# Kernel tuning notes

Measured on AMD Instinct MI355X. Metric: run time of the kernel, lower is better.

## Reference

```python
import jax, jax.numpy as jnp
import numpy as np

EMBED_DIM = 1024
CONTEXT_LEN = 2048
NUM_HEADS = 16
HEAD_DIM = EMBED_DIM // NUM_HEADS
BATCH = 2
SEQ = 2048


def setup_inputs() -> dict:
    key = jax.random.key(0)
    ks = jax.random.split(key, 6)
    s = 1.0 / np.sqrt(EMBED_DIM)
    x = jax.random.normal(ks[0], (BATCH, SEQ, EMBED_DIM), dtype=jnp.float32)
    # nn.Linear weights stored as [out, in]; we keep [in, out] for x @ W
    W_q = jax.random.uniform(ks[1], (EMBED_DIM, EMBED_DIM), jnp.float32, -s, s)
    W_k = jax.random.uniform(ks[2], (EMBED_DIM, EMBED_DIM), jnp.float32, -s, s)
    W_v = jax.random.uniform(ks[3], (EMBED_DIM, EMBED_DIM), jnp.float32, -s, s)
    W_o = jax.random.uniform(ks[4], (EMBED_DIM, EMBED_DIM), jnp.float32, -s, s)
    b_o = jax.random.uniform(ks[5], (EMBED_DIM,), jnp.float32, -s, s)
    return {"x": x, "W_q": W_q, "W_k": W_k, "W_v": W_v, "W_o": W_o, "b_o": b_o}


def reference(x, W_q, W_k, W_v, W_o, b_o):
    b, s, _ = x.shape
    # project and split heads: [b, s, e] -> [b, h, s, d]
    def heads(t):
        return t.reshape(b, s, NUM_HEADS, HEAD_DIM).transpose(0, 2, 1, 3)
    q = heads(x @ W_q)
    k = heads(x @ W_k)
    v = heads(x @ W_v)
    scores = jnp.einsum("bhqd,bhkd->bhqk", q, k)  # full seq x seq scores
    causal = jnp.triu(jnp.ones((s, s), dtype=bool), k=1)
    scores = jnp.where(causal, -jnp.inf, scores)
    attn = jax.nn.softmax(scores / np.sqrt(HEAD_DIM).astype(np.float32), axis=-1)
    ctx = jnp.einsum("bhqk,bhkd->bhqd", attn, v)
    ctx = ctx.transpose(0, 2, 1, 3).reshape(b, s, EMBED_DIM)
    return ctx @ W_o + b_o
```

## Files before the change

### kernel.cpp

```cpp
#include <hip/hip_runtime.h>

#define EMBED 1024
#define SEQL  2048
#define NHEAD 16
#define HDIM  64
#define NBATCH 2
#define MROWS 4096

typedef __attribute__((ext_vector_type(4))) float  f32x4;
typedef __attribute__((ext_vector_type(8))) __bf16 bf16x8;

__device__ __forceinline__ short f2bf(float f){
  union { float f; unsigned u; } x; x.f = f;
  unsigned r = x.u + 0x7fffu + ((x.u >> 16) & 1u);
  return (short)(r >> 16);
}

#define GLDS(gp, lp) __builtin_amdgcn_global_load_lds( \
    (const __attribute__((address_space(1))) void*)(gp), \
    (__attribute__((address_space(3))) void*)(lp), 16, 0, 0)

__global__ __launch_bounds__(256) void cvt_kernel(const float* __restrict__ in,
                                                  short* __restrict__ out, int n){
  int i = (blockIdx.x * 256 + threadIdx.x) * 4;
  if (i >= n) return;
  float4 v = *(const float4*)(in + i);
  short4 o; o.x = f2bf(v.x); o.y = f2bf(v.y); o.z = f2bf(v.z); o.w = f2bf(v.w);
  *(short4*)(out + i) = o;
}

__global__ __launch_bounds__(256) void transpose_kernel(const float* __restrict__ W0,
    const float* __restrict__ W1, const float* __restrict__ W2, const float* __restrict__ W3,
    short* __restrict__ WtAll){
  __shared__ float tile[32][33];
  const int z = blockIdx.z;
  const float* W = (z==0)?W0:(z==1)?W1:(z==2)?W2:W3;
  short* Wt = WtAll + z*(EMBED*EMBED);
  const int bx = blockIdx.x*32, by = blockIdx.y*32;
  const int tx = threadIdx.x & 31, ty = threadIdx.x >> 5;
  #pragma unroll
  for (int i=0;i<32;i+=8) tile[ty+i][tx] = W[(by+ty+i)*EMBED + bx+tx];
  __syncthreads();
  #pragma unroll
  for (int i=0;i<32;i+=8) Wt[(bx+ty+i)*EMBED + by+tx] = f2bf(tile[tx][ty+i]);
}

__device__ __forceinline__ void gemm_tile_128(const short* __restrict__ A,
    const short* __restrict__ Bt, short* As, short* Bs, int m0, int n0, f32x4 acc[4][4]){
  const int tid  = threadIdx.x;
  const int lane = tid & 63;
  const int wid  = tid >> 6;
  const int wrow = (wid >> 1) * 64, wcol = (wid & 1) * 64;
  const int arow = tid >> 2, acol8 = (tid & 3) * 8;
  const int l15 = lane & 15, lg = lane >> 4;

  auto STAGE = [&](int b, int k0){
    short* as = As + b*4096;
    short* bs = Bs + b*4096;
    GLDS(A  + (m0      + arow) * 1024 + k0 + acol8, as + tid*8);
    GLDS(A  + (m0 + 64 + arow) * 1024 + k0 + acol8, as + 2048 + tid*8);
    GLDS(Bt + (n0      + arow) * 1024 + k0 + acol8, bs + tid*8);
    GLDS(Bt + (n0 + 64 + arow) * 1024 + k0 + acol8, bs + 2048 + tid*8);
  };

  STAGE(0, 0);
  __syncthreads();
  int cur = 0;
  for (int k0 = 0; k0 < 1024; k0 += 32){
    if (k0 + 32 < 1024) STAGE(cur ^ 1, k0 + 32);
    const short* as = As + cur*4096;
    const short* bs = Bs + cur*4096;
    bf16x8 a[4], b[4];
    #pragma unroll
    for (int i=0;i<4;++i) a[i] = *(const bf16x8*)(as + (wrow+16*i+l15)*32 + 8*lg);
    #pragma unroll
    for (int j=0;j<4;++j) b[j] = *(const bf16x8*)(bs + (wcol+16*j+l15)*32 + 8*lg);
    #pragma unroll
    for (int i=0;i<4;++i)
      #pragma unroll
      for (int j=0;j<4;++j)
        acc[i][j] = __builtin_amdgcn_mfma_f32_16x16x32_bf16(a[i], b[j], acc[i][j], 0,0,0);
    __syncthreads();
    cur ^= 1;
  }
}

__device__ __forceinline__ void gemm_tile_64(const short* __restrict__ A,
    const short* __restrict__ Bt, short* As, short* Bs, int m0, int n0, f32x4 acc[2][4]){
  const int tid  = threadIdx.x;
  const int lane = tid & 63;
  const int wid  = tid >> 6;
  const int wrow = (wid >> 1) * 32, wcol = (wid & 1) * 64;
  const int arow = tid >> 2, acol8 = (tid & 3) * 8;
  const int l15 = lane & 15, lg = lane >> 4;

  auto STAGE = [&](int b, int k0){
    short* as = As + b*2048;
    short* bs = Bs + b*4096;
    GLDS(A  + (m0      + arow) * 1024 + k0 + acol8, as + tid*8);
    GLDS(Bt + (n0      + arow) * 1024 + k0 + acol8, bs + tid*8);
    GLDS(Bt + (n0 + 64 + arow) * 1024 + k0 + acol8, bs + 2048 + tid*8);
  };

  STAGE(0, 0);
  __syncthreads();
  int cur = 0;
  for (int k0 = 0; k0 < 1024; k0 += 32){
    if (k0 + 32 < 1024) STAGE(cur ^ 1, k0 + 32);
    const short* as = As + cur*2048;
    const short* bs = Bs + cur*4096;
    bf16x8 a[2], b[4];
    #pragma unroll
    for (int i=0;i<2;++i) a[i] = *(const bf16x8*)(as + (wrow+16*i+l15)*32 + 8*lg);
    #pragma unroll
    for (int j=0;j<4;++j) b[j] = *(const bf16x8*)(bs + (wcol+16*j+l15)*32 + 8*lg);
    #pragma unroll
    for (int i=0;i<2;++i)
      #pragma unroll
      for (int j=0;j<4;++j)
        acc[i][j] = __builtin_amdgcn_mfma_f32_16x16x32_bf16(a[i], b[j], acc[i][j], 0,0,0);
    __syncthreads();
    cur ^= 1;
  }
}

__global__ __launch_bounds__(256) void gemm_qkv_kernel(const short* __restrict__ Xb,
    const short* __restrict__ WtAll, short* __restrict__ Q, short* __restrict__ K,
    short* __restrict__ Vt){
  __shared__ __align__(16) short SH[16384];
  short* As = SH;
  short* Bs = SH + 8192;
  const int m0 = blockIdx.x*128, n0 = blockIdx.y*128, z = blockIdx.z;
  const short* Bt = WtAll + z*(EMBED*EMBED);
  f32x4 acc[4][4] = {};
  gemm_tile_128(Xb, Bt, As, Bs, m0, n0, acc);
  const int tid  = threadIdx.x;
  const int lane = tid & 63;
  const int wid  = tid >> 6;
  const int wrow = (wid >> 1) * 64, wcol = (wid & 1) * 64;
  const int l15 = lane & 15, lg = lane >> 4;
  const int bb = m0 >> 11, srow0 = m0 & 2047;

  if (z < 2){
    short* out = z ? K : Q;
    const float qscl = (z==0) ? (0.125f * 1.44269504f) : 1.0f;
    #pragma unroll
    for (int i=0;i<4;++i)
      #pragma unroll
      for (int j=0;j<4;++j)
        #pragma unroll
        for (int r=0;r<4;++r){
          int m = m0 + wrow + 16*i + 4*lg + r;
          int n = n0 + wcol + 16*j + l15;
          int srow = m & 2047, hh = n >> 6, d = n & 63;
          out[(((bb<<4)+hh)*SEQL + srow)*HDIM + d] = f2bf(acc[i][j][r] * qscl);
        }
  } else {
    short* T = SH;
    #pragma unroll
    for (int i=0;i<4;++i)
      #pragma unroll
      for (int j=0;j<4;++j){
        int n_loc = wcol + 16*j + l15;
        int mb    = wrow + 16*i + 4*lg;
        short4 pk;
        pk.x = f2bf(acc[i][j][0]); pk.y = f2bf(acc[i][j][1]);
        pk.z = f2bf(acc[i][j][2]); pk.w = f2bf(acc[i][j][3]);
        *(short4*)(T + n_loc*128 + (mb ^ ((n_loc & 7) << 3))) = pk;
      }
    __syncthreads();
    #pragma unroll
    for (int it=0; it<8; ++it){
      int n_loc = 16*it + (tid >> 4);
      int mch   = (tid & 15) * 8;
      int4 v = *(const int4*)(T + n_loc*128 + (mch ^ ((n_loc & 7) << 3)));
      int n_glob = n0 + n_loc;
      int hh = n_glob >> 6, d = n_glob & 63;
      *(int4*)(Vt + (((bb<<4)+hh)*HDIM + d)*SEQL + srow0 + mch) = v;
    }
  }
}

__global__ __launch_bounds__(256) void gemm_out_kernel(const short* __restrict__ Ctx,
    const short* __restrict__ WtO, const float* __restrict__ bias, float* __restrict__ out){
  __shared__ __align__(16) short As[2*2048], Bs[2*4096];
  const int m0 = blockIdx.x*64, n0 = blockIdx.y*128;
  f32x4 acc[2][4] = {};
  gemm_tile_64(Ctx, WtO, As, Bs, m0, n0, acc);
  const int lane = threadIdx.x & 63;
  const int wid  = threadIdx.x >> 6;
  const int wrow = (wid >> 1) * 32, wcol = (wid & 1) * 64;
  const int l15 = lane & 15, lg = lane >> 4;
  #pragma unroll
  for (int i=0;i<2;++i)
    #pragma unroll
    for (int j=0;j<4;++j)
      #pragma unroll
      for (int r=0;r<4;++r){
        int m = m0 + wrow + 16*i + 4*lg + r;
        int n = n0 + wcol + 16*j + l15;
        out[m*EMBED + n] = acc[i][j][r] + bias[n];
      }
}

__global__ __launch_bounds__(512, 4) void attn_kernel(const short* __restrict__ Q,
    const short* __restrict__ K, const short* __restrict__ Vt, short* __restrict__ Ctx){
  __shared__ __align__(16) char lds[49152];
  const int tid  = threadIdx.x;
  const int lane = tid & 63;
  const int wid  = tid >> 6;
  const int bid   = blockIdx.x;
  const int xcd   = bid & 7;
  const int i7    = bid >> 3;
  const int bh    = xcd + 8*(i7 & 3);
  const int cidx  = i7 >> 2;
  const int chunk = (cidx < 8) ? cidx : 23 - cidx;
  const int q0blk = chunk * 128;
  const int ntblk = 2*chunk + 2;
  const int q0w   = q0blk + 16*wid;
  const int qlast = q0w + 15;

  const short* Qh  = Q  + bh*(SEQL*HDIM);
  const char*  KhB = (const char*)(K  + bh*(SEQL*HDIM));
  const char*  VhB = (const char*)(Vt + bh*(HDIM*SEQL));
  const int l15 = lane & 15, lg = lane >> 4;
  const int lg20 = 20 * lg;
  const int swE = (l15 & 7) << 3;
  const int swB = (l15 & 7) << 4;
  const int laneRow = lane >> 3;
  const int colSwz  = 16 * ((lane & 7) ^ laneRow);
  const int r0 = 8 * wid;

  const short* qp = Qh + (q0w + l15)*HDIM + 8*lg;
  bf16x8 bq0 = *(const bf16x8*)qp;
  bf16x8 bq1 = *(const bf16x8*)(qp + 32);

  f32x4 acc[4];
  #pragma unroll
  for (int j=0; j<4; ++j) acc[j] = (f32x4){0.f,0.f,0.f,0.f};
  float mrun = -3e30f, lrun = 0.f;

  short* pw = (short*)(lds + 32768 + wid*2048);

  auto STAGE = [&](int b, int t){
    char* kb = lds + b*16384;
    char* vb = kb + 8192;
    const int kv0 = t*64;
    GLDS(KhB + (kv0 + r0 + laneRow)*128 + colSwz, kb + r0*128);
    GLDS(VhB + (r0 + laneRow)*4096 + kv0*2 + colSwz, vb + r0*128);
  };

  STAGE(0, 0);
  __syncthreads();

  int cur = 0;
  for (int t = 0; t < ntblk; ++t){
    const int kv0 = t*64;
    if (t + 1 < ntblk) STAGE(cur ^ 1, t + 1);
    if (kv0 <= qlast){
      const char* kb = lds + cur*16384;
      const char* vb = kb + 8192;
      f32x4 sc[4];
      __builtin_amdgcn_s_setprio(1);
      #pragma unroll
      for (int c=0; c<4; ++c){
        const char* kr = kb + (16*c + l15)*128;
        bf16x8 k0 = *(const bf16x8*)(kr + ((16*lg) ^ swB));
        bf16x8 k1 = *(const bf16x8*)(kr + ((64 + 16*lg) ^ swB));
        f32x4 z = (f32x4){0.f,0.f,0.f,0.f};
        z = __builtin_amdgcn_mfma_f32_16x16x32_bf16(k0, bq0, z, 0,0,0);
        z = __builtin_amdgcn_mfma_f32_16x16x32_bf16(k1, bq1, z, 0,0,0);
        sc[c] = z;
      }
      __builtin_amdgcn_s_setprio(0);
      if (kv0 + 63 > q0w){
        #pragma unroll
        for (int c=0; c<4; ++c)
          #pragma unroll
          for (int r=0; r<4; ++r)
            if (kv0 + 16*c + 4*lg + r > q0w + l15) sc[c][r] = -3e30f;
      }
      float pm = -3e30f;
      #pragma unroll
      for (int c=0; c<4; ++c)
        #pragma unroll
        for (int r=0; r<4; ++r) pm = fmaxf(pm, sc[c][r]);
      pm = fmaxf(pm, __shfl_xor(pm, 16));
      pm = fmaxf(pm, __shfl_xor(pm, 32));
      const int resc = !__all(pm <= mrun);
      float mn = mrun, ss = 1.0f;
      if (resc){
        mn = fmaxf(mrun, pm);
        ss = __builtin_amdgcn_exp2f(mrun - mn);
        mrun = mn;
      }
      float ls = 0.f;
      #pragma unroll
      for (int c=0; c<4; ++c)
        #pragma unroll
        for (int r=0; r<4; ++r){
          float p = __builtin_amdgcn_exp2f(sc[c][r] - mn);
          sc[c][r] = p;
          ls += p;
        }
      ls += __shfl_xor(ls, 16);
      ls += __shfl_xor(ls, 32);
      if (resc){
        lrun = lrun*ss + ls;
        float srg[4];
        #pragma unroll
        for (int r=0; r<4; ++r) srg[r] = __shfl(ss, lg20 + r);
        #pragma unroll
        for (int j=0; j<4; ++j)
          #pragma unroll
          for (int r=0; r<4; ++r) acc[j][r] *= srg[r];
      } else {
        lrun += ls;
      }
      #pragma unroll
      for (int c=0; c<4; ++c){
        short4 pk;
        pk.x = f2bf(sc[c][0]); pk.y = f2bf(sc[c][1]);
        pk.z = f2bf(sc[c][2]); pk.w = f2bf(sc[c][3]);
        *(short4*)(pw + l15*64 + ((16*c + 4*lg) ^ swE)) = pk;
      }
      bf16x8 pa0 = *(const bf16x8*)(pw + l15*64 + ((8*lg)      ^ swE));
      bf16x8 pa1 = *(const bf16x8*)(pw + l15*64 + ((32 + 8*lg) ^ swE));
      __builtin_amdgcn_s_setprio(1);
      #pragma unroll
      for (int j=0; j<4; ++j){
        const char* vrp = vb + (16*j + l15)*128;
        bf16x8 v0 = *(const bf16x8*)(vrp + ((16*lg) ^ swB));
        bf16x8 v1 = *(const bf16x8*)(vrp + ((64 + 16*lg) ^ swB));
        acc[j] = __builtin_amdgcn_mfma_f32_16x16x32_bf16(pa0, v0, acc[j], 0,0,0);
        acc[j] = __builtin_amdgcn_mfma_f32_16x16x32_bf16(pa1, v1, acc[j], 0,0,0);
      }
      __builtin_amdgcn_s_setprio(0);
    }
    __syncthreads();
    cur ^= 1;
  }

  const int bb = bh >> 4, hh = bh & 15;
  float lr[4];
  #pragma unroll
  for (int r=0; r<4; ++r) lr[r] = __builtin_amdgcn_rcpf(__shfl(lrun, lg20 + r));
  #pragma unroll
  for (int j=0; j<4; ++j)
    #pragma unroll
    for (int r=0; r<4; ++r){
      int qg = q0w + 4*lg + r;
      Ctx[(bb*SEQL + qg)*EMBED + hh*HDIM + 16*j + l15] = f2bf(acc[j][r] * lr[r]);
    }
}

extern "C" void kernel_launch(void* const* d_in, const int* in_sizes, int n_in,
                              void* d_out, int out_size, void* d_ws, size_t ws_size,
                              hipStream_t stream){
  const float* x  = (const float*)d_in[0];
  const float* Wq = (const float*)d_in[1];
  const float* Wk = (const float*)d_in[2];
  const float* Wv = (const float*)d_in[3];
  const float* Wo = (const float*)d_in[4];
  const float* bo = (const float*)d_in[5];
  float* out = (float*)d_out;

  char* ws = (char*)d_ws;
  const size_t MB = 1u << 20;
  short* Xb  = (short*)(ws +  0*MB);
  short* Wt  = (short*)(ws +  8*MB);
  short* Q   = (short*)(ws + 16*MB);
  short* Kk  = (short*)(ws + 24*MB);
  short* Vt  = (short*)(ws + 32*MB);
  short* Ctx = (short*)(ws + 40*MB);

  cvt_kernel<<<4096, 256, 0, stream>>>(x, Xb, MROWS*EMBED);
  transpose_kernel<<<dim3(32,32,4), 256, 0, stream>>>(Wq, Wk, Wv, Wo, Wt);
  gemm_qkv_kernel<<<dim3(32,8,3), 256, 0, stream>>>(Xb, Wt, Q, Kk, Vt);
  attn_kernel<<<512, 512, 0, stream>>>(Q, Kk, Vt, Ctx);
  gemm_out_kernel<<<dim3(64,8), 256, 0, stream>>>(Ctx, Wt + 3*(EMBED*EMBED), bo, out);
}
```

Before: 112.2 us.

## Use triple-buffered LDS pipelines with explicit vmcnt waits; merge prep kernels

Switches the GEMM and attention main loops from double to triple buffering. Each loop keeps two global-to-LDS stages in flight and waits on a partial vmcnt plus a raw s_barrier instead of a full __syncthreads drain. The cvt and transpose kernels are merged into one prep launch, saving one kernel launch. The extra LDS (64KB per attention block) may reduce occupancy, and correctness depends on the vmcnt counts matching the number of loads issued per stage.

```diff
diff --git a/kernel.cpp b/kernel.cpp
--- a/kernel.cpp
+++ b/kernel.cpp
@@ -20,29 +20,34 @@
     (const __attribute__((address_space(1))) void*)(gp), \
     (__attribute__((address_space(3))) void*)(lp), 16, 0, 0)
 
-__global__ __launch_bounds__(256) void cvt_kernel(const float* __restrict__ in,
-                                                  short* __restrict__ out, int n){
-  int i = (blockIdx.x * 256 + threadIdx.x) * 4;
-  if (i >= n) return;
-  float4 v = *(const float4*)(in + i);
-  short4 o; o.x = f2bf(v.x); o.y = f2bf(v.y); o.z = f2bf(v.z); o.w = f2bf(v.w);
-  *(short4*)(out + i) = o;
-}
-
-__global__ __launch_bounds__(256) void transpose_kernel(const float* __restrict__ W0,
-    const float* __restrict__ W1, const float* __restrict__ W2, const float* __restrict__ W3,
-    short* __restrict__ WtAll){
+#define WAITV(N) do { asm volatile("s_waitcnt vmcnt(" #N ")" ::: "memory"); \
+                      __builtin_amdgcn_sched_barrier(0); } while(0)
+#define BARRIER() do { __builtin_amdgcn_s_barrier(); \
+                       __builtin_amdgcn_sched_barrier(0); } while(0)
+
+__global__ __launch_bounds__(256) void prep_kernel(const float* __restrict__ x,
+    const float* __restrict__ W0, const float* __restrict__ W1,
+    const float* __restrict__ W2, const float* __restrict__ W3,
+    short* __restrict__ Xb, short* __restrict__ WtAll){
   __shared__ float tile[32][33];
   const int z = blockIdx.z;
-  const float* W = (z==0)?W0:(z==1)?W1:(z==2)?W2:W3;
-  short* Wt = WtAll + z*(EMBED*EMBED);
-  const int bx = blockIdx.x*32, by = blockIdx.y*32;
-  const int tx = threadIdx.x & 31, ty = threadIdx.x >> 5;
-  #pragma unroll
-  for (int i=0;i<32;i+=8) tile[ty+i][tx] = W[(by+ty+i)*EMBED + bx+tx];
-  __syncthreads();
-  #pragma unroll
-  for (int i=0;i<32;i+=8) Wt[(bx+ty+i)*EMBED + by+tx] = f2bf(tile[tx][ty+i]);
+  if (z < 4){
+    const float* W = (z==0)?W0:(z==1)?W1:(z==2)?W2:W3;
+    short* Wt = WtAll + z*(EMBED*EMBED);
+    const int bx = blockIdx.x*32, by = blockIdx.y*32;
+    const int tx = threadIdx.x & 31, ty = threadIdx.x >> 5;
+    #pragma unroll
+    for (int i=0;i<32;i+=8) tile[ty+i][tx] = W[(by+ty+i)*EMBED + bx+tx];
+    __syncthreads();
+    #pragma unroll
+    for (int i=0;i<32;i+=8) Wt[(bx+ty+i)*EMBED + by+tx] = f2bf(tile[tx][ty+i]);
+  } else {
+    const int blk = (z-4)*1024 + blockIdx.y*32 + blockIdx.x;
+    const int i = (blk*256 + threadIdx.x)*4;
+    float4 v = *(const float4*)(x + i);
+    short4 o; o.x=f2bf(v.x); o.y=f2bf(v.y); o.z=f2bf(v.z); o.w=f2bf(v.w);
+    *(short4*)(Xb + i) = o;
+  }
 }
 
 __device__ __forceinline__ void gemm_tile_128(const short* __restrict__ A,
@@ -63,13 +68,13 @@
     GLDS(Bt + (n0 + 64 + arow) * 1024 + k0 + acol8, bs + 2048 + tid*8);
   };
 
-  STAGE(0, 0);
-  __syncthreads();
-  int cur = 0;
-  for (int k0 = 0; k0 < 1024; k0 += 32){
-    if (k0 + 32 < 1024) STAGE(cur ^ 1, k0 + 32);
-    const short* as = As + cur*4096;
-    const short* bs = Bs + cur*4096;
+  STAGE(0, 0); STAGE(1, 32);
+  WAITV(4);
+  BARRIER();
+  for (int k = 0; k < 32; ++k){
+    if (k + 2 < 32) STAGE((k+2)%3, (k+2)*32);
+    const short* as = As + (k%3)*4096;
+    const short* bs = Bs + (k%3)*4096;
     bf16x8 a[4], b[4];
     #pragma unroll
     for (int i=0;i<4;++i) a[i] = *(const bf16x8*)(as + (wrow+16*i+l15)*32 + 8*lg);
@@ -80,8 +85,8 @@
       #pragma unroll
       for (int j=0;j<4;++j)
         acc[i][j] = __builtin_amdgcn_mfma_f32_16x16x32_bf16(a[i], b[j], acc[i][j], 0,0,0);
-    __syncthreads();
-    cur ^= 1;
+    if (k + 2 < 32) { WAITV(4); } else { WAITV(0); }
+    BARRIER();
   }
 }
 
@@ -102,13 +107,13 @@
     GLDS(Bt + (n0 + 64 + arow) * 1024 + k0 + acol8, bs + 2048 + tid*8);
   };
 
-  STAGE(0, 0);
-  __syncthreads();
-  int cur = 0;
-  for (int k0 = 0; k0 < 1024; k0 += 32){
-    if (k0 + 32 < 1024) STAGE(cur ^ 1, k0 + 32);
-    const short* as = As + cur*2048;
-    const short* bs = Bs + cur*4096;
+  STAGE(0, 0); STAGE(1, 32);
+  WAITV(3);
+  BARRIER();
+  for (int k = 0; k < 32; ++k){
+    if (k + 2 < 32) STAGE((k+2)%3, (k+2)*32);
+    const short* as = As + (k%3)*2048;
+    const short* bs = Bs + (k%3)*4096;
     bf16x8 a[2], b[4];
     #pragma unroll
     for (int i=0;i<2;++i) a[i] = *(const bf16x8*)(as + (wrow+16*i+l15)*32 + 8*lg);
@@ -119,17 +124,17 @@
       #pragma unroll
       for (int j=0;j<4;++j)
         acc[i][j] = __builtin_amdgcn_mfma_f32_16x16x32_bf16(a[i], b[j], acc[i][j], 0,0,0);
-    __syncthreads();
-    cur ^= 1;
+    if (k + 2 < 32) { WAITV(3); } else { WAITV(0); }
+    BARRIER();
   }
 }
 
 __global__ __launch_bounds__(256) void gemm_qkv_kernel(const short* __restrict__ Xb,
     const short* __restrict__ WtAll, short* __restrict__ Q, short* __restrict__ K,
     short* __restrict__ Vt){
-  __shared__ __align__(16) short SH[16384];
+  __shared__ __align__(16) short SH[24576];
   short* As = SH;
-  short* Bs = SH + 8192;
+  short* Bs = SH + 12288;
   const int m0 = blockIdx.x*128, n0 = blockIdx.y*128, z = blockIdx.z;
   const short* Bt = WtAll + z*(EMBED*EMBED);
   f32x4 acc[4][4] = {};
@@ -183,7 +188,7 @@
 
 __global__ __launch_bounds__(256) void gemm_out_kernel(const short* __restrict__ Ctx,
     const short* __restrict__ WtO, const float* __restrict__ bias, float* __restrict__ out){
-  __shared__ __align__(16) short As[2*2048], Bs[2*4096];
+  __shared__ __align__(16) short As[3*2048], Bs[3*4096];
   const int m0 = blockIdx.x*64, n0 = blockIdx.y*128;
   f32x4 acc[2][4] = {};
   gemm_tile_64(Ctx, WtO, As, Bs, m0, n0, acc);
@@ -205,7 +210,7 @@
 
 __global__ __launch_bounds__(512, 4) void attn_kernel(const short* __restrict__ Q,
     const short* __restrict__ K, const short* __restrict__ Vt, short* __restrict__ Ctx){
-  __shared__ __align__(16) char lds[49152];
+  __shared__ __align__(16) char lds[65536];
   const int tid  = threadIdx.x;
   const int lane = tid & 63;
   const int wid  = tid >> 6;
@@ -240,7 +245,7 @@
   for (int j=0; j<4; ++j) acc[j] = (f32x4){0.f,0.f,0.f,0.f};
   float mrun = -3e30f, lrun = 0.f;
 
-  short* pw = (short*)(lds + 32768 + wid*2048);
+  short* pw = (short*)(lds + 49152 + wid*2048);
 
   auto STAGE = [&](int b, int t){
     char* kb = lds + b*16384;
@@ -250,15 +255,15 @@
     GLDS(VhB + (r0 + laneRow)*4096 + kv0*2 + colSwz, vb + r0*128);
   };
 
-  STAGE(0, 0);
-  __syncthreads();
-
-  int cur = 0;
+  STAGE(0, 0); STAGE(1, 1);
+  WAITV(2);
+  BARRIER();
+
   for (int t = 0; t < ntblk; ++t){
     const int kv0 = t*64;
-    if (t + 1 < ntblk) STAGE(cur ^ 1, t + 1);
+    if (t + 2 < ntblk) STAGE((t+2)%3, t+2);
     if (kv0 <= qlast){
-      const char* kb = lds + cur*16384;
+      const char* kb = lds + (t%3)*16384;
       const char* vb = kb + 8192;
       f32x4 sc[4];
       __builtin_amdgcn_s_setprio(1);
@@ -337,8 +342,8 @@
       }
       __builtin_amdgcn_s_setprio(0);
     }
-    __syncthreads();
-    cur ^= 1;
+    if (t + 2 < ntblk) { WAITV(2); } else { WAITV(0); }
+    BARRIER();
   }
 
   const int bb = bh >> 4, hh = bh & 15;
@@ -374,8 +379,7 @@
   short* Vt  = (short*)(ws + 32*MB);
   short* Ctx = (short*)(ws + 40*MB);
 
-  cvt_kernel<<<4096, 256, 0, stream>>>(x, Xb, MROWS*EMBED);
-  transpose_kernel<<<dim3(32,32,4), 256, 0, stream>>>(Wq, Wk, Wv, Wo, Wt);
+  prep_kernel<<<dim3(32,32,8), 256, 0, stream>>>(x, Wq, Wk, Wv, Wo, Xb, Wt);
   gemm_qkv_kernel<<<dim3(32,8,3), 256, 0, stream>>>(Xb, Wt, Q, Kk, Vt);
   attn_kernel<<<512, 512, 0, stream>>>(Q, Kk, Vt, Ctx);
   gemm_out_kernel<<<dim3(64,8), 256, 0, stream>>>(Ctx, Wt + 3*(EMBED*EMBED), bo, out);
```

Result: no change. 112.8 us (+0.5%).
